# Optimization experiments

Hardware: AMD Instinct MI355X
Metric: run time of the kernel (lower is better)

Reference implementation:

```python
import jax, jax.numpy as jnp
import numpy as np

BETA = 1.0
EPS = 1e-8  # matches torch F.cosine_similarity eps


def setup_inputs() -> dict:
    key = jax.random.key(0)
    x = jax.random.normal(key, (4096, 2, 1024), dtype=jnp.float32)
    return {"x": x}


def _cosine_sim_matrix(pos, anc):
    # pos: [B, D], anc: [B, D] -> [B, B], sim[i, j] = cos(pos[i], anc[j])
    dots = jnp.einsum('id,jd->ij', pos, anc)
    pn = jnp.sqrt(jnp.sum(pos * pos, axis=-1))
    an = jnp.sqrt(jnp.sum(anc * anc, axis=-1))
    denom = jnp.maximum(pn[:, None] * an[None, :], EPS)
    return dots / denom


def reference(x):
    # x: [B, M, D], M >= 2
    out_anchor = jnp.mean(x[:, 1:, :], axis=1)   # [B, D]
    out_positive = x[:, 0, :]                     # [B, D]
    sim = _cosine_sim_matrix(out_positive, out_anchor)  # [B, B]
    n = sim.shape[0]

    diag = jnp.diagonal(sim)                      # [B]
    # tempsim for column i: beta * (sim[:, i] - sim[i, i]), excluding row i
    T = BETA * (sim - diag[None, :])              # [B, B]
    eye = jnp.eye(n, dtype=bool)

    # exclude-diagonal logsumexp per column (vectorized over all columns)
    Tm = jnp.where(eye, -jnp.inf, T)
    temploss = jax.nn.logsumexp(Tm, axis=0)       # [B]
    # flatNCE trick: exp(l - stop_grad(l)) has value 1 but gradient of l
    nloss = jnp.mean(jnp.exp(temploss - jax.lax.stop_gradient(temploss)))

    # top-1 accuracy against labels arange(B) (detached in original)
    label = jnp.arange(n)
    prec1 = jnp.mean((jnp.argmax(sim, axis=1) == label).astype(jnp.float32)) * 100.0
    return nloss, prec1
```

## Files before the change

kernel.cpp:

```cpp
#include <hip/hip_runtime.h>


#define NROWS 4096
#define DDIM  1024
#define XSTR  2048

typedef unsigned int u32;
typedef unsigned long long u64;
typedef __attribute__((ext_vector_type(8))) short bf16x8;
typedef __attribute__((ext_vector_type(16))) float f32x16;

__device__ __forceinline__ unsigned int fkey(float f) {
    unsigned int u = __float_as_uint(f);
    return (u & 0x80000000u) ? ~u : (u | 0x80000000u);
}

__device__ __forceinline__ u64 shfl_xor_u64(u64 v, int m) {
    unsigned int lo = (unsigned int)v;
    unsigned int hi = (unsigned int)(v >> 32);
    lo = __shfl_xor(lo, m, 64);
    hi = __shfl_xor(hi, m, 64);
    return ((u64)hi << 32) | lo;
}

__device__ __forceinline__ unsigned short f2bf(float f) {
    unsigned u = __float_as_uint(f);
    return (unsigned short)((u + 0x7FFFu + ((u >> 16) & 1u)) >> 16);
}

#define PF_OFF   0u
#define AF_OFF   8388608u
#define INV_OFF  16777216u
#define PCK_OFF  16793600u
#define DONE_OFF 16826368u
#define WS_NEED  16826432u

__global__ __launch_bounds__(256) void norms2_kernel(const float* __restrict__ x,
                                                     float* __restrict__ inv_an,
                                                     u64* __restrict__ packed,
                                                     unsigned int* __restrict__ done) {
    int gid  = blockIdx.x * 256 + threadIdx.x;
    int j    = gid >> 6;
    int lane = threadIdx.x & 63;
    if (gid < NROWS) packed[gid] = 0ULL;
    if (gid == 0) *done = 0u;
    const float4* a = (const float4*)(x + (size_t)j * XSTR + DDIM);
    float s = 0.0f;
#pragma unroll
    for (int i = 0; i < 4; ++i) {
        float4 v = a[lane + i * 64];
        s += v.x * v.x + v.y * v.y + v.z * v.z + v.w * v.w;
    }
#pragma unroll
    for (int off = 32; off > 0; off >>= 1) s += __shfl_down(s, off, 64);
    if (lane == 0) inv_an[j] = 1.0f / sqrtf(s);
}

__global__ __launch_bounds__(256) void conv_kernel(const float* __restrict__ x,
                                                   unsigned short* __restrict__ Pf,
                                                   unsigned short* __restrict__ Af) {
    const int cid  = blockIdx.x * 256 + threadIdx.x;
    const int lane = cid & 63;
    const int kh   = (cid >> 6) & 63;
    const int b    = cid >> 12;
    const int row  = b * 32 + (lane & 31);
    const int col  = kh * 16 + (lane >> 5) * 8;

    const float* px = x + (size_t)row * XSTR + col;
    float4 p0 = *(const float4*)(px);
    float4 p1 = *(const float4*)(px + 4);
    float4 a0 = *(const float4*)(px + DDIM);
    float4 a1 = *(const float4*)(px + DDIM + 4);

    ushort4* pd = (ushort4*)(Pf + (size_t)cid * 8);
    ushort4* ad = (ushort4*)(Af + (size_t)cid * 8);
    pd[0] = make_ushort4(f2bf(p0.x), f2bf(p0.y), f2bf(p0.z), f2bf(p0.w));
    pd[1] = make_ushort4(f2bf(p1.x), f2bf(p1.y), f2bf(p1.z), f2bf(p1.w));
    ad[0] = make_ushort4(f2bf(a0.x), f2bf(a0.y), f2bf(a0.z), f2bf(a0.w));
    ad[1] = make_ushort4(f2bf(a1.x), f2bf(a1.y), f2bf(a1.z), f2bf(a1.w));
}

#define FRAG(base, blk, kh) (*(const bf16x8*)((base) + (((size_t)(blk)) << 16) + ((kh) << 10)))

__global__ __launch_bounds__(512, 2) void mfma_gemm_argmax(const unsigned short* __restrict__ Pf,
                                                           const unsigned short* __restrict__ Af,
                                                           const float* __restrict__ inv_an,
                                                           u64* __restrict__ packed,
                                                           unsigned int* __restrict__ done,
                                                           float* __restrict__ out) {
    __shared__ unsigned int lastflag;
    __shared__ int cnt[8];

    const int bid = blockIdx.x;
    const int xcd = bid & 7;
    const int slt = bid >> 3;
    const int rblk = (xcd >> 1) * 4 + (slt >> 3);
    const int cblk = (xcd & 1) * 8 + (slt & 7);
    const int r0 = rblk * 256;
    const int c0 = cblk * 256;

    const int wave = threadIdx.x >> 6;
    const int lane = threadIdx.x & 63;
    const int l31 = lane & 31;
    const int lh = lane >> 5;
    const int wm = wave & 3;
    const int wn = wave >> 2;

    const int mb0 = rblk * 8 + wm * 2;
    const int nb0 = cblk * 8 + wn * 4;

    const char* pP = (const char*)Pf + (size_t)lane * 16 + ((size_t)mb0 << 16);
    const char* pA = (const char*)Af + (size_t)lane * 16 + ((size_t)nb0 << 16);

    f32x16 zero16 = {0.f,0.f,0.f,0.f,0.f,0.f,0.f,0.f,0.f,0.f,0.f,0.f,0.f,0.f,0.f,0.f};
    f32x16 acc[2][4];
#pragma unroll
    for (int i = 0; i < 2; ++i)
#pragma unroll
        for (int j = 0; j < 4; ++j) acc[i][j] = zero16;

    bf16x8 ph[3][2], aa[3][4];
#pragma unroll
    for (int q = 0; q < 2; ++q) { ph[0][q] = FRAG(pP, q, 0); ph[1][q] = FRAG(pP, q, 1); }
#pragma unroll
    for (int q = 0; q < 4; ++q) { aa[0][q] = FRAG(pA, q, 0); aa[1][q] = FRAG(pA, q, 1); }

#pragma unroll
    for (int kh = 0; kh < 64; ++kh) {
        const int cs = kh % 3;
        if (kh + 2 < 64) {
            const int ns = (kh + 2) % 3;
#pragma unroll
            for (int q = 0; q < 2; ++q) ph[ns][q] = FRAG(pP, q, kh + 2);
#pragma unroll
            for (int q = 0; q < 4; ++q) aa[ns][q] = FRAG(pA, q, kh + 2);
        }
#pragma unroll
        for (int mt = 0; mt < 2; ++mt)
#pragma unroll
            for (int nt = 0; nt < 4; ++nt)
                acc[mt][nt] = __builtin_amdgcn_mfma_f32_32x32x16_bf16(ph[cs][mt], aa[cs][nt], acc[mt][nt], 0, 0, 0);
    }

    float ian[4];
#pragma unroll
    for (int nt = 0; nt < 4; ++nt) ian[nt] = inv_an[c0 + wn * 128 + nt * 32 + l31];

#pragma unroll
    for (int mt = 0; mt < 2; ++mt)
#pragma unroll
        for (int reg = 0; reg < 16; ++reg) {
            const int row = r0 + wm * 64 + mt * 32 + (reg & 3) + 8 * (reg >> 2) + 4 * lh;
            u64 best = 0ULL;
#pragma unroll
            for (int nt = 0; nt < 4; ++nt) {
                const int col = c0 + wn * 128 + nt * 32 + l31;
                const float v = acc[mt][nt][reg] * ian[nt];
                const u64 p = ((u64)fkey(v) << 32) | (unsigned int)(~col);
                best = best > p ? best : p;
            }
#pragma unroll
            for (int m = 1; m <= 16; m <<= 1) {
                const u64 o = shfl_xor_u64(best, m);
                best = best > o ? best : o;
            }
            if (l31 == 0) atomicMax(&packed[row], best);
        }

    __syncthreads();
    if (threadIdx.x == 0) {
        __threadfence();
        unsigned int old = atomicAdd(done, 1u);
        lastflag = (old == 255u) ? 1u : 0u;
    }
    __syncthreads();
    if (lastflag) {
        int c = 0;
        for (int r = threadIdx.x; r < NROWS; r += 512) {
            u64 v = atomicAdd(&packed[r], 0ULL);
            unsigned int col = ~(unsigned int)(v & 0xFFFFFFFFULL);
            c += (col == (unsigned int)r) ? 1 : 0;
        }
#pragma unroll
        for (int off = 32; off > 0; off >>= 1) c += __shfl_down(c, off, 64);
        if ((threadIdx.x & 63) == 0) cnt[threadIdx.x >> 6] = c;
        __syncthreads();
        if (threadIdx.x == 0) {
            int tot = 0;
#pragma unroll
            for (int w = 0; w < 8; ++w) tot += cnt[w];
            out[0] = 1.0f;
            out[1] = 100.0f * (float)tot / (float)NROWS;
        }
    }
}

__global__ __launch_bounds__(256) void norms_kernel(const float* __restrict__ x,
                                                    float* __restrict__ inv_an,
                                                    u64* __restrict__ packed) {
    int gid  = blockIdx.x * 256 + threadIdx.x;
    int j    = gid >> 6;
    int lane = threadIdx.x & 63;
    if (gid < NROWS) packed[gid] = 0ULL;
    const float4* a = (const float4*)(x + (size_t)j * XSTR + DDIM);
    float s = 0.0f;
#pragma unroll
    for (int i = 0; i < 4; ++i) {
        float4 v = a[lane + i * 64];
        s += v.x * v.x + v.y * v.y + v.z * v.z + v.w * v.w;
    }
#pragma unroll
    for (int off = 32; off > 0; off >>= 1) s += __shfl_down(s, off, 64);
    if (lane == 0) inv_an[j] = 1.0f / sqrtf(s);
}

__global__ __launch_bounds__(256) void gemm_argmax_kernel(const float* __restrict__ x,
                                                          const float* __restrict__ inv_an,
                                                          u64* __restrict__ packed) {
    __shared__ __align__(16) float Pt[16][128];
    __shared__ __align__(16) float At[16][128];
    const int r0 = blockIdx.x * 128;
    const int c0 = blockIdx.y * 128;
    const int t = threadIdx.x;
    const int tx = t & 15;
    const int ty = t >> 4;
    const int srow = t >> 1;
    const int skq = (t & 1) * 8;
    float acc[8][8];
#pragma unroll
    for (int r = 0; r < 8; ++r)
#pragma unroll
        for (int c = 0; c < 8; ++c) acc[r][c] = 0.0f;
    const float* gp = x + (size_t)(r0 + srow) * XSTR + skq;
    const float* ga = x + (size_t)(c0 + srow) * XSTR + DDIM + skq;
    for (int k0 = 0; k0 < DDIM; k0 += 16) {
        __syncthreads();
        float4 p0 = *(const float4*)(gp + k0);
        float4 p1 = *(const float4*)(gp + k0 + 4);
        float4 a0 = *(const float4*)(ga + k0);
        float4 a1 = *(const float4*)(ga + k0 + 4);
        Pt[skq + 0][srow] = p0.x; Pt[skq + 1][srow] = p0.y;
        Pt[skq + 2][srow] = p0.z; Pt[skq + 3][srow] = p0.w;
        Pt[skq + 4][srow] = p1.x; Pt[skq + 5][srow] = p1.y;
        Pt[skq + 6][srow] = p1.z; Pt[skq + 7][srow] = p1.w;
        At[skq + 0][srow] = a0.x; At[skq + 1][srow] = a0.y;
        At[skq + 2][srow] = a0.z; At[skq + 3][srow] = a0.w;
        At[skq + 4][srow] = a1.x; At[skq + 5][srow] = a1.y;
        At[skq + 6][srow] = a1.z; At[skq + 7][srow] = a1.w;
        __syncthreads();
#pragma unroll
        for (int kk = 0; kk < 16; ++kk) {
            float pr[8], ar[8];
            *(float4*)&pr[0] = *(const float4*)&Pt[kk][ty * 8];
            *(float4*)&pr[4] = *(const float4*)&Pt[kk][ty * 8 + 4];
            *(float4*)&ar[0] = *(const float4*)&At[kk][tx * 8];
            *(float4*)&ar[4] = *(const float4*)&At[kk][tx * 8 + 4];
#pragma unroll
            for (int r = 0; r < 8; ++r)
#pragma unroll
                for (int c = 0; c < 8; ++c) acc[r][c] += pr[r] * ar[c];
        }
    }
    float ian[8];
#pragma unroll
    for (int c = 0; c < 8; ++c) ian[c] = inv_an[c0 + tx * 8 + c];
#pragma unroll
    for (int r = 0; r < 8; ++r) {
        int row = r0 + ty * 8 + r;
        u64 best = 0ULL;
#pragma unroll
        for (int c = 0; c < 8; ++c) {
            int col = c0 + tx * 8 + c;
            float v = acc[r][c] * ian[c];
            u64 p = ((u64)fkey(v) << 32) | (unsigned int)(~col);
            best = best > p ? best : p;
        }
#pragma unroll
        for (int m = 1; m <= 8; m <<= 1) {
            u64 o = shfl_xor_u64(best, m);
            best = best > o ? best : o;
        }
        if (tx == 0) atomicMax(&packed[row], best);
    }
}

__global__ __launch_bounds__(256) void finalize_kernel(const u64* __restrict__ packed,
                                                       float* __restrict__ out) {
    __shared__ int cnt_s;
    int t = threadIdx.x;
    if (t == 0) cnt_s = 0;
    __syncthreads();
    int c = 0;
    for (int r = t; r < NROWS; r += 256) {
        unsigned int col = ~(unsigned int)(packed[r] & 0xFFFFFFFFULL);
        c += (col == (unsigned int)r) ? 1 : 0;
    }
#pragma unroll
    for (int off = 32; off > 0; off >>= 1) c += __shfl_down(c, off, 64);
    if ((t & 63) == 0) atomicAdd(&cnt_s, c);
    __syncthreads();
    if (t == 0) {
        out[0] = 1.0f;
        out[1] = 100.0f * (float)cnt_s / (float)NROWS;
    }
}

extern "C" void kernel_launch(void* const* d_in, const int* in_sizes, int n_in,
                              void* d_out, int out_size, void* d_ws, size_t ws_size,
                              hipStream_t stream) {
    (void)in_sizes; (void)n_in; (void)out_size;
    const float* x = (const float*)d_in[0];
    float* out = (float*)d_out;

    if (ws_size >= (size_t)WS_NEED) {
        char* ws = (char*)d_ws;
        unsigned short* Pf = (unsigned short*)(ws + PF_OFF);
        unsigned short* Af = (unsigned short*)(ws + AF_OFF);
        float* inv_an = (float*)(ws + INV_OFF);
        u64* packed = (u64*)(ws + PCK_OFF);
        unsigned int* done = (unsigned int*)(ws + DONE_OFF);

        norms2_kernel<<<NROWS / 4, 256, 0, stream>>>(x, inv_an, packed, done);
        conv_kernel<<<2048, 256, 0, stream>>>(x, Pf, Af);
        mfma_gemm_argmax<<<256, 512, 0, stream>>>(Pf, Af, inv_an, packed, done, out);
    } else {
        float* inv_an = (float*)d_ws;
        u64* packed = (u64*)((char*)d_ws + NROWS * sizeof(float));
        norms_kernel<<<NROWS / 4, 256, 0, stream>>>(x, inv_an, packed);
        dim3 grid(NROWS / 128, NROWS / 128);
        gemm_argmax_kernel<<<grid, 256, 0, stream>>>(x, inv_an, packed);
        finalize_kernel<<<1, 256, 0, stream>>>(packed, out);
    }
}
```

Baseline: 131.4 us.

## Fuse norms, bf16 conversion, GEMM-argmax and finalize into one cooperative kernel

Replaces the three-kernel sequence (norm computation, bf16 fragment conversion, MFMA GEMM with argmax) with a single cooperative launch. The phases are separated by grid-wide syncs, and block 0 does the final accuracy reduction after the last sync. This removes two kernel launch gaps and the done-counter based finalize. In exchange it adds grid.sync overhead and requires all 256 blocks to be co-resident. If the cooperative launch fails, it falls back to the old path.

```diff
diff --git a/kernel.cpp b/kernel.cpp
--- a/kernel.cpp
+++ b/kernel.cpp
@@ -1,5 +1,8 @@
 #include <hip/hip_runtime.h>
-
+#include <hip/hip_cooperative_groups.h>
+
+
+namespace cg = cooperative_groups;
 
 #define NROWS 4096
 #define DDIM  1024
@@ -8,6 +11,7 @@
 typedef unsigned int u32;
 typedef unsigned long long u64;
 typedef __attribute__((ext_vector_type(8))) short bf16x8;
+typedef __attribute__((ext_vector_type(8))) unsigned short u16x8;
 typedef __attribute__((ext_vector_type(16))) float f32x16;
 
 __device__ __forceinline__ unsigned int fkey(float f) {
@@ -34,6 +38,169 @@
 #define PCK_OFF  16793600u
 #define DONE_OFF 16826368u
 #define WS_NEED  16826432u
+
+#define FRAG(base, blk, kh) (*(const bf16x8*)((base) + (((size_t)(blk)) << 16) + ((kh) << 10)))
+
+__device__ __forceinline__ void conv_chunk(const float* __restrict__ x,
+                                           unsigned short* __restrict__ Pf,
+                                           unsigned short* __restrict__ Af, int cid) {
+    const int lane = cid & 63;
+    const int kh   = (cid >> 6) & 63;
+    const int fb   = cid >> 12;
+    const int row  = fb * 32 + (lane & 31);
+    const int col  = kh * 16 + (lane >> 5) * 8;
+
+    const float* px = x + (size_t)row * XSTR + col;
+    float4 p0 = *(const float4*)(px);
+    float4 p1 = *(const float4*)(px + 4);
+    float4 a0 = *(const float4*)(px + DDIM);
+    float4 a1 = *(const float4*)(px + DDIM + 4);
+
+    u16x8 pv, av;
+    pv[0] = f2bf(p0.x); pv[1] = f2bf(p0.y); pv[2] = f2bf(p0.z); pv[3] = f2bf(p0.w);
+    pv[4] = f2bf(p1.x); pv[5] = f2bf(p1.y); pv[6] = f2bf(p1.z); pv[7] = f2bf(p1.w);
+    av[0] = f2bf(a0.x); av[1] = f2bf(a0.y); av[2] = f2bf(a0.z); av[3] = f2bf(a0.w);
+    av[4] = f2bf(a1.x); av[5] = f2bf(a1.y); av[6] = f2bf(a1.z); av[7] = f2bf(a1.w);
+
+    *(u16x8*)(Pf + (size_t)cid * 8) = pv;
+    *(u16x8*)(Af + (size_t)cid * 8) = av;
+}
+
+__global__ __launch_bounds__(512, 2) void fused_all(const float* __restrict__ x,
+                                                    unsigned short* __restrict__ Pf,
+                                                    unsigned short* __restrict__ Af,
+                                                    float* __restrict__ inv_an,
+                                                    u64* __restrict__ packed,
+                                                    float* __restrict__ out) {
+    __shared__ int cnt[8];
+    cg::grid_group grid = cg::this_grid();
+
+    const int b = blockIdx.x;
+    const int t = threadIdx.x;
+    const int wave = t >> 6;
+    const int lane = t & 63;
+
+    if (t < 16) packed[b * 16 + t] = 0ULL;
+
+#pragma unroll
+    for (int rr = 0; rr < 2; ++rr) {
+        const int row = b * 16 + wave * 2 + rr;
+        const float4* a = (const float4*)(x + (size_t)row * XSTR + DDIM);
+        float s = 0.0f;
+#pragma unroll
+        for (int i = 0; i < 4; ++i) {
+            float4 v = a[lane + i * 64];
+            s += v.x * v.x + v.y * v.y + v.z * v.z + v.w * v.w;
+        }
+#pragma unroll
+        for (int off = 32; off > 0; off >>= 1) s += __shfl_down(s, off, 64);
+        if (lane == 0) inv_an[row] = 1.0f / sqrtf(s);
+    }
+
+#pragma unroll
+    for (int i = 0; i < 4; ++i) conv_chunk(x, Pf, Af, b * 2048 + i * 512 + t);
+
+    __threadfence();
+    grid.sync();
+    __threadfence();
+
+    const int bid = b;
+    const int xcd = bid & 7;
+    const int slt = bid >> 3;
+    const int rblk = (xcd >> 1) * 4 + (slt >> 3);
+    const int cblk = (xcd & 1) * 8 + (slt & 7);
+    const int r0 = rblk * 256;
+    const int c0 = cblk * 256;
+
+    const int l31 = lane & 31;
+    const int lh = lane >> 5;
+    const int wm = wave & 3;
+    const int wn = wave >> 2;
+
+    const int mb0 = rblk * 8 + wm * 2;
+    const int nb0 = cblk * 8 + wn * 4;
+
+    const char* pP = (const char*)Pf + (size_t)lane * 16 + ((size_t)mb0 << 16);
+    const char* pA = (const char*)Af + (size_t)lane * 16 + ((size_t)nb0 << 16);
+
+    f32x16 zero16 = {0.f,0.f,0.f,0.f,0.f,0.f,0.f,0.f,0.f,0.f,0.f,0.f,0.f,0.f,0.f,0.f};
+    f32x16 acc[2][4];
+#pragma unroll
+    for (int i = 0; i < 2; ++i)
+#pragma unroll
+        for (int j = 0; j < 4; ++j) acc[i][j] = zero16;
+
+    bf16x8 ph[3][2], aa[3][4];
+#pragma unroll
+    for (int q = 0; q < 2; ++q) { ph[0][q] = FRAG(pP, q, 0); ph[1][q] = FRAG(pP, q, 1); }
+#pragma unroll
+    for (int q = 0; q < 4; ++q) { aa[0][q] = FRAG(pA, q, 0); aa[1][q] = FRAG(pA, q, 1); }
+
+#pragma unroll
+    for (int kh = 0; kh < 64; ++kh) {
+        const int cs = kh % 3;
+        if (kh + 2 < 64) {
+            const int ns = (kh + 2) % 3;
+#pragma unroll
+            for (int q = 0; q < 2; ++q) ph[ns][q] = FRAG(pP, q, kh + 2);
+#pragma unroll
+            for (int q = 0; q < 4; ++q) aa[ns][q] = FRAG(pA, q, kh + 2);
+        }
+#pragma unroll
+        for (int mt = 0; mt < 2; ++mt)
+#pragma unroll
+            for (int nt = 0; nt < 4; ++nt)
+                acc[mt][nt] = __builtin_amdgcn_mfma_f32_32x32x16_bf16(ph[cs][mt], aa[cs][nt], acc[mt][nt], 0, 0, 0);
+    }
+
+    float ian[4];
+#pragma unroll
+    for (int nt = 0; nt < 4; ++nt) ian[nt] = inv_an[c0 + wn * 128 + nt * 32 + l31];
+
+#pragma unroll
+    for (int mt = 0; mt < 2; ++mt)
+#pragma unroll
+        for (int reg = 0; reg < 16; ++reg) {
+            const int row = r0 + wm * 64 + mt * 32 + (reg & 3) + 8 * (reg >> 2) + 4 * lh;
+            u64 best = 0ULL;
+#pragma unroll
+            for (int nt = 0; nt < 4; ++nt) {
+                const int col = c0 + wn * 128 + nt * 32 + l31;
+                const float v = acc[mt][nt][reg] * ian[nt];
+                const u64 p = ((u64)fkey(v) << 32) | (unsigned int)(~col);
+                best = best > p ? best : p;
+            }
+#pragma unroll
+            for (int m = 1; m <= 16; m <<= 1) {
+                const u64 o = shfl_xor_u64(best, m);
+                best = best > o ? best : o;
+            }
+            if (l31 == 0) atomicMax(&packed[row], best);
+        }
+
+    __threadfence();
+    grid.sync();
+    if (b == 0) {
+        __threadfence();
+        int c = 0;
+        for (int r = t; r < NROWS; r += 512) {
+            u64 v = atomicAdd(&packed[r], 0ULL);
+            unsigned int col = ~(unsigned int)(v & 0xFFFFFFFFULL);
+            c += (col == (unsigned int)r) ? 1 : 0;
+        }
+#pragma unroll
+        for (int off = 32; off > 0; off >>= 1) c += __shfl_down(c, off, 64);
+        if (lane == 0) cnt[wave] = c;
+        __syncthreads();
+        if (t == 0) {
+            int tot = 0;
+#pragma unroll
+            for (int w = 0; w < 8; ++w) tot += cnt[w];
+            out[0] = 1.0f;
+            out[1] = 100.0f * (float)tot / (float)NROWS;
+        }
+    }
+}
 
 __global__ __launch_bounds__(256) void norms2_kernel(const float* __restrict__ x,
                                                      float* __restrict__ inv_an,
@@ -59,28 +226,9 @@
 __global__ __launch_bounds__(256) void conv_kernel(const float* __restrict__ x,
                                                    unsigned short* __restrict__ Pf,
                                                    unsigned short* __restrict__ Af) {
-    const int cid  = blockIdx.x * 256 + threadIdx.x;
-    const int lane = cid & 63;
-    const int kh   = (cid >> 6) & 63;
-    const int b    = cid >> 12;
-    const int row  = b * 32 + (lane & 31);
-    const int col  = kh * 16 + (lane >> 5) * 8;
-
-    const float* px = x + (size_t)row * XSTR + col;
-    float4 p0 = *(const float4*)(px);
-    float4 p1 = *(const float4*)(px + 4);
-    float4 a0 = *(const float4*)(px + DDIM);
-    float4 a1 = *(const float4*)(px + DDIM + 4);
-
-    ushort4* pd = (ushort4*)(Pf + (size_t)cid * 8);
-    ushort4* ad = (ushort4*)(Af + (size_t)cid * 8);
-    pd[0] = make_ushort4(f2bf(p0.x), f2bf(p0.y), f2bf(p0.z), f2bf(p0.w));
-    pd[1] = make_ushort4(f2bf(p1.x), f2bf(p1.y), f2bf(p1.z), f2bf(p1.w));
-    ad[0] = make_ushort4(f2bf(a0.x), f2bf(a0.y), f2bf(a0.z), f2bf(a0.w));
-    ad[1] = make_ushort4(f2bf(a1.x), f2bf(a1.y), f2bf(a1.z), f2bf(a1.w));
-}
-
-#define FRAG(base, blk, kh) (*(const bf16x8*)((base) + (((size_t)(blk)) << 16) + ((kh) << 10)))
+    const int cid = blockIdx.x * 256 + threadIdx.x;
+    conv_chunk(x, Pf, Af, cid);
+}
 
 __global__ __launch_bounds__(512, 2) void mfma_gemm_argmax(const unsigned short* __restrict__ Pf,
                                                            const unsigned short* __restrict__ Af,
@@ -320,9 +468,15 @@
         u64* packed = (u64*)(ws + PCK_OFF);
         unsigned int* done = (unsigned int*)(ws + DONE_OFF);
 
-        norms2_kernel<<<NROWS / 4, 256, 0, stream>>>(x, inv_an, packed, done);
-        conv_kernel<<<2048, 256, 0, stream>>>(x, Pf, Af);
-        mfma_gemm_argmax<<<256, 512, 0, stream>>>(Pf, Af, inv_an, packed, done, out);
+        void* args[] = {(void*)&x, (void*)&Pf, (void*)&Af,
+                        (void*)&inv_an, (void*)&packed, (void*)&out};
+        hipError_t e = hipLaunchCooperativeKernel((void*)fused_all, dim3(256), dim3(512),
+                                                  args, 0, stream);
+        if (e != hipSuccess) {
+            norms2_kernel<<<NROWS / 4, 256, 0, stream>>>(x, inv_an, packed, done);
+            conv_kernel<<<2048, 256, 0, stream>>>(x, Pf, Af);
+            mfma_gemm_argmax<<<256, 512, 0, stream>>>(Pf, Af, inv_an, packed, done, out);
+        }
     } else {
         float* inv_an = (float*)d_ws;
         u64* packed = (u64*)((char*)d_ws + NROWS * sizeof(float));
```

Result: slower. 327.9 us (+149.6%).

## Stage GEMM fragments through LDS with direct global-to-LDS double buffering

Applied to the files above, without the earlier changes.

Each wave of the GEMM kernel used to load its own bf16 fragments from global memory into registers, so each block fetched its row and column panels several times over. Now the block loads each panel once into a double-buffered LDS tile using global_load_lds, and waves read their fragments from LDS, with barriers and setprio around the MFMA bursts. The conversion kernel also writes one 16-byte vector instead of two 8-byte stores. The cost is 128KB of LDS per block, which may limit occupancy against the launch bound of two blocks, plus several barriers on every k-step.

```diff
diff --git a/kernel.cpp b/kernel.cpp
--- a/kernel.cpp
+++ b/kernel.cpp
@@ -8,6 +8,7 @@
 typedef unsigned int u32;
 typedef unsigned long long u64;
 typedef __attribute__((ext_vector_type(8))) short bf16x8;
+typedef __attribute__((ext_vector_type(8))) unsigned short u16x8;
 typedef __attribute__((ext_vector_type(16))) float f32x16;
 
 __device__ __forceinline__ unsigned int fkey(float f) {
@@ -62,8 +63,8 @@
     const int cid  = blockIdx.x * 256 + threadIdx.x;
     const int lane = cid & 63;
     const int kh   = (cid >> 6) & 63;
-    const int b    = cid >> 12;
-    const int row  = b * 32 + (lane & 31);
+    const int fb   = cid >> 12;
+    const int row  = fb * 32 + (lane & 31);
     const int col  = kh * 16 + (lane >> 5) * 8;
 
     const float* px = x + (size_t)row * XSTR + col;
@@ -72,15 +73,15 @@
     float4 a0 = *(const float4*)(px + DDIM);
     float4 a1 = *(const float4*)(px + DDIM + 4);
 
-    ushort4* pd = (ushort4*)(Pf + (size_t)cid * 8);
-    ushort4* ad = (ushort4*)(Af + (size_t)cid * 8);
-    pd[0] = make_ushort4(f2bf(p0.x), f2bf(p0.y), f2bf(p0.z), f2bf(p0.w));
-    pd[1] = make_ushort4(f2bf(p1.x), f2bf(p1.y), f2bf(p1.z), f2bf(p1.w));
-    ad[0] = make_ushort4(f2bf(a0.x), f2bf(a0.y), f2bf(a0.z), f2bf(a0.w));
-    ad[1] = make_ushort4(f2bf(a1.x), f2bf(a1.y), f2bf(a1.z), f2bf(a1.w));
-}
-
-#define FRAG(base, blk, kh) (*(const bf16x8*)((base) + (((size_t)(blk)) << 16) + ((kh) << 10)))
+    u16x8 pv, av;
+    pv[0] = f2bf(p0.x); pv[1] = f2bf(p0.y); pv[2] = f2bf(p0.z); pv[3] = f2bf(p0.w);
+    pv[4] = f2bf(p1.x); pv[5] = f2bf(p1.y); pv[6] = f2bf(p1.z); pv[7] = f2bf(p1.w);
+    av[0] = f2bf(a0.x); av[1] = f2bf(a0.y); av[2] = f2bf(a0.z); av[3] = f2bf(a0.w);
+    av[4] = f2bf(a1.x); av[5] = f2bf(a1.y); av[6] = f2bf(a1.z); av[7] = f2bf(a1.w);
+
+    *(u16x8*)(Pf + (size_t)cid * 8) = pv;
+    *(u16x8*)(Af + (size_t)cid * 8) = av;
+}
 
 __global__ __launch_bounds__(512, 2) void mfma_gemm_argmax(const unsigned short* __restrict__ Pf,
                                                            const unsigned short* __restrict__ Af,
@@ -88,6 +89,7 @@
                                                            u64* __restrict__ packed,
                                                            unsigned int* __restrict__ done,
                                                            float* __restrict__ out) {
+    __shared__ __align__(16) unsigned int lds[32768];
     __shared__ unsigned int lastflag;
     __shared__ int cnt[8];
 
@@ -106,11 +108,8 @@
     const int wm = wave & 3;
     const int wn = wave >> 2;
 
-    const int mb0 = rblk * 8 + wm * 2;
-    const int nb0 = cblk * 8 + wn * 4;
-
-    const char* pP = (const char*)Pf + (size_t)lane * 16 + ((size_t)mb0 << 16);
-    const char* pA = (const char*)Af + (size_t)lane * 16 + ((size_t)nb0 << 16);
+    const char* gPs = (const char*)Pf + (((size_t)(rblk * 8 + wave)) << 16) + (size_t)lane * 16;
+    const char* gAs = (const char*)Af + (((size_t)(cblk * 8 + wave)) << 16) + (size_t)lane * 16;
 
     f32x16 zero16 = {0.f,0.f,0.f,0.f,0.f,0.f,0.f,0.f,0.f,0.f,0.f,0.f,0.f,0.f,0.f,0.f};
     f32x16 acc[2][4];
@@ -119,27 +118,57 @@
 #pragma unroll
         for (int j = 0; j < 4; ++j) acc[i][j] = zero16;
 
-    bf16x8 ph[3][2], aa[3][4];
-#pragma unroll
-    for (int q = 0; q < 2; ++q) { ph[0][q] = FRAG(pP, q, 0); ph[1][q] = FRAG(pP, q, 1); }
-#pragma unroll
-    for (int q = 0; q < 4; ++q) { aa[0][q] = FRAG(pA, q, 0); aa[1][q] = FRAG(pA, q, 1); }
-
-#pragma unroll
-    for (int kh = 0; kh < 64; ++kh) {
-        const int cs = kh % 3;
-        if (kh + 2 < 64) {
-            const int ns = (kh + 2) % 3;
-#pragma unroll
-            for (int q = 0; q < 2; ++q) ph[ns][q] = FRAG(pP, q, kh + 2);
-#pragma unroll
-            for (int q = 0; q < 4; ++q) aa[ns][q] = FRAG(pA, q, kh + 2);
-        }
-#pragma unroll
-        for (int mt = 0; mt < 2; ++mt)
-#pragma unroll
-            for (int nt = 0; nt < 4; ++nt)
-                acc[mt][nt] = __builtin_amdgcn_mfma_f32_32x32x16_bf16(ph[cs][mt], aa[cs][nt], acc[mt][nt], 0, 0, 0);
+#pragma unroll
+    for (int kh_l = 0; kh_l < 4; ++kh_l) {
+        __builtin_amdgcn_global_load_lds((const u32*)(gPs + ((size_t)kh_l << 10)),
+                                         &lds[kh_l * 2048 + wave * 256], 16, 0, 0);
+        __builtin_amdgcn_global_load_lds((const u32*)(gAs + ((size_t)kh_l << 10)),
+                                         &lds[8192 + kh_l * 2048 + wave * 256], 16, 0, 0);
+    }
+
+    for (int t = 0; t < 16; ++t) {
+        const int cb = t & 1;
+        const int nbuf = (cb ^ 1) * 16384;
+        const int cbuf = cb * 16384;
+
+        asm volatile("s_waitcnt vmcnt(0)" ::: "memory");
+        __builtin_amdgcn_s_barrier();
+        __builtin_amdgcn_sched_barrier(0);
+
+#pragma unroll
+        for (int kh_l = 0; kh_l < 4; ++kh_l) {
+            const u32* bp = &lds[cbuf + kh_l * 2048 + (wm * 2) * 256 + lane * 4];
+            bf16x8 f_p0 = *(const bf16x8*)(bp);
+            bf16x8 f_p1 = *(const bf16x8*)(bp + 256);
+            const u32* ba = &lds[cbuf + 8192 + kh_l * 2048 + (wn * 4) * 256 + lane * 4];
+            bf16x8 f_a0 = *(const bf16x8*)(ba);
+            bf16x8 f_a1 = *(const bf16x8*)(ba + 256);
+            bf16x8 f_a2 = *(const bf16x8*)(ba + 512);
+            bf16x8 f_a3 = *(const bf16x8*)(ba + 768);
+
+            if (t + 1 < 16) {
+                const size_t go = ((size_t)((t + 1) * 4 + kh_l)) << 10;
+                __builtin_amdgcn_global_load_lds((const u32*)(gPs + go),
+                                                 &lds[nbuf + kh_l * 2048 + wave * 256], 16, 0, 0);
+                __builtin_amdgcn_global_load_lds((const u32*)(gAs + go),
+                                                 &lds[nbuf + 8192 + kh_l * 2048 + wave * 256], 16, 0, 0);
+            }
+
+            __builtin_amdgcn_s_barrier();
+            asm volatile("s_waitcnt lgkmcnt(0)" ::: "memory");
+            __builtin_amdgcn_sched_barrier(0);
+            __builtin_amdgcn_s_setprio(1);
+            acc[0][0] = __builtin_amdgcn_mfma_f32_32x32x16_bf16(f_p0, f_a0, acc[0][0], 0, 0, 0);
+            acc[0][1] = __builtin_amdgcn_mfma_f32_32x32x16_bf16(f_p0, f_a1, acc[0][1], 0, 0, 0);
+            acc[0][2] = __builtin_amdgcn_mfma_f32_32x32x16_bf16(f_p0, f_a2, acc[0][2], 0, 0, 0);
+            acc[0][3] = __builtin_amdgcn_mfma_f32_32x32x16_bf16(f_p0, f_a3, acc[0][3], 0, 0, 0);
+            acc[1][0] = __builtin_amdgcn_mfma_f32_32x32x16_bf16(f_p1, f_a0, acc[1][0], 0, 0, 0);
+            acc[1][1] = __builtin_amdgcn_mfma_f32_32x32x16_bf16(f_p1, f_a1, acc[1][1], 0, 0, 0);
+            acc[1][2] = __builtin_amdgcn_mfma_f32_32x32x16_bf16(f_p1, f_a2, acc[1][2], 0, 0, 0);
+            acc[1][3] = __builtin_amdgcn_mfma_f32_32x32x16_bf16(f_p1, f_a3, acc[1][3], 0, 0, 0);
+            __builtin_amdgcn_s_setprio(0);
+            __builtin_amdgcn_s_barrier();
+        }
     }
 
     float ian[4];
```

New measurement: 123.3 us. 1.07x faster.
